# Kernel optimization log

Hardware: AMD Instinct MI355X
Metric: run time of the kernel (lower is better)

## Reference

```python
import jax, jax.numpy as jnp
import numpy as np

N, E, D, R = 50000, 800000, 128, 16
NUM_OBJS, NUM_ATTRS, L = 179, 10, 5
OBJ_DIM, ATTR_DIM, HID, NANGLE = 96, 32, 512, 24


def setup_inputs() -> dict:
    key = jax.random.key(0)
    ks = jax.random.split(key, 20)
    z = jax.random.normal(ks[0], (N, D), dtype=jnp.float32)
    objs = jax.random.randint(ks[1], (N,), 0, NUM_OBJS + 1)
    s = jax.random.randint(ks[2], (E,), 0, N)
    o = jax.random.randint(ks[3], (E,), 0, N)
    p = jax.random.randint(ks[4], (E,), 0, R)
    triples = jnp.stack([s, p, o], axis=1)
    attributes = jax.random.randint(ks[5], (N,), 0, NUM_ATTRS)
    w = 0.05
    obj_emb = jax.random.normal(ks[6], (NUM_OBJS + 1, OBJ_DIM), dtype=jnp.float32)
    attr_emb = jax.random.normal(ks[7], (NUM_ATTRS, ATTR_DIM), dtype=jnp.float32)
    Wrel = jax.random.normal(ks[8], (L, R, D, D), dtype=jnp.float32) * w
    Wroot = jax.random.normal(ks[9], (L, D, D), dtype=jnp.float32) * w
    bconv = jnp.zeros((L, D), dtype=jnp.float32)
    box_W1 = jax.random.normal(ks[10], (2 * D + ATTR_DIM, HID), dtype=jnp.float32) * w
    box_b1 = jnp.zeros((HID,), dtype=jnp.float32)
    box_W2 = jax.random.normal(ks[11], (HID, 6), dtype=jnp.float32) * w
    box_b2 = jnp.zeros((6,), dtype=jnp.float32)
    ang_W1 = jax.random.normal(ks[12], (2 * D, HID), dtype=jnp.float32) * w
    ang_b1 = jnp.zeros((HID,), dtype=jnp.float32)
    ang_W2 = jax.random.normal(ks[13], (HID, NANGLE), dtype=jnp.float32) * w
    ang_b2 = jnp.zeros((NANGLE,), dtype=jnp.float32)
    return dict(z=z, objs=objs, triples=triples, attributes=attributes,
                obj_emb=obj_emb, attr_emb=attr_emb, Wrel=Wrel, Wroot=Wroot,
                bconv=bconv, box_W1=box_W1, box_b1=box_b1, box_W2=box_W2,
                box_b2=box_b2, ang_W1=ang_W1, ang_b1=ang_b1, ang_W2=ang_W2,
                ang_b2=ang_b2)


def _rgcn_layer(x, s, o, p, Wr, Wroot_l, b):
    # relation-typed transform of all nodes: [N, R, D]
    h_rel = jnp.einsum('nd,rdf->nrf', x, Wr)
    msgs = h_rel[s, p]                                   # [E, D] gather
    # mean aggregation per (target, relation), as in PyG RGCNConv
    seg = o * R + p
    cnt = jax.ops.segment_sum(jnp.ones((s.shape[0],), x.dtype), seg,
                              num_segments=x.shape[0] * R)
    deg = jnp.maximum(cnt[seg], 1.0)
    agg = jax.ops.segment_sum(msgs / deg[:, None], o, num_segments=x.shape[0])
    return x @ Wroot_l + agg + b


def reference(z, objs, triples, attributes, obj_emb, attr_emb, Wrel, Wroot,
              bconv, box_W1, box_b1, box_W2, box_b2, ang_W1, ang_b1,
              ang_W2, ang_b2):
    s, p, o = triples[:, 0], triples[:, 1], triples[:, 2]
    attr_vecs = attr_emb[attributes]                     # [N, 32]
    obj_vecs = jnp.concatenate([obj_emb[objs], attr_vecs], axis=1)  # [N, 128]
    for j in range(L):
        obj_vecs = jax.nn.relu(_rgcn_layer(obj_vecs, s, o, p,
                                           Wrel[j], Wroot[j], bconv[j]))
    obj_vecs = jnp.concatenate([obj_vecs, z], axis=1)    # [N, 256]
    obj_vecs_box = jnp.concatenate([obj_vecs, attr_vecs], axis=1)  # [N, 288]
    boxes_pred = jax.nn.relu(obj_vecs_box @ box_W1 + box_b1) @ box_W2 + box_b2
    ang_h = jax.nn.relu(obj_vecs @ ang_W1 + ang_b1) @ ang_W2 + ang_b2
    angles_pred = jax.nn.log_softmax(ang_h, axis=1)
    return boxes_pred, angles_pred
```

## Files before the change

### kernel.cpp

```cpp
#include <hip/hip_runtime.h>
#include <hip/hip_bf16.h>
#include <math.h>

#define NN   50000
#define EE   800000
#define RREL 16
#define LLAY 5
#define NBINS (NN * RREL)
#define HCAP 565248

typedef __attribute__((ext_vector_type(8))) short s8v;
typedef __attribute__((ext_vector_type(4))) float f4v;

__device__ __forceinline__ unsigned short f2bf(float f) {
  __hip_bfloat16 h = __float2bfloat16(f);
  return __builtin_bit_cast(unsigned short, h);
}
__device__ __forceinline__ float bf2f(unsigned int u) {
  return __builtin_bit_cast(float, u << 16);
}
__device__ __forceinline__ void split1(float v, unsigned short& h, unsigned short& l) {
  __hip_bfloat16 hb = __float2bfloat16(v);
  float hf = __bfloat162float(hb);
  h = __builtin_bit_cast(unsigned short, hb);
  __hip_bfloat16 lb = __float2bfloat16(v - hf);
  l = __builtin_bit_cast(unsigned short, lb);
}

__global__ void build_x0_kernel(const int* __restrict__ objs, const int* __restrict__ attrs,
                                const float* __restrict__ obj_emb, const float* __restrict__ attr_emb,
                                unsigned short* __restrict__ xh) {
  int t = blockIdx.x * blockDim.x + threadIdx.x;
  if (t >= NN * 32) return;
  int n = t >> 5, q = t & 31;
  float4 v;
  if (q < 24) v = *(const float4*)&obj_emb[(size_t)objs[n] * 96 + q * 4];
  else        v = *(const float4*)&attr_emb[(size_t)attrs[n] * 32 + (q - 24) * 4];
  ushort4 h;
  h.x = f2bf(v.x); h.y = f2bf(v.y); h.z = f2bf(v.z); h.w = f2bf(v.w);
  *(ushort4*)&xh[(size_t)n * 128 + q * 4] = h;
}

__global__ void prep_zattr(const float* __restrict__ z, const int* __restrict__ attrs,
                           const float* __restrict__ attr_emb,
                           unsigned short* __restrict__ zh, unsigned short* __restrict__ ah) {
  int t = blockIdx.x * blockDim.x + threadIdx.x;
  if (t >= NN * 40) return;
  int n = t / 40, q = t % 40;
  float4 v;
  ushort4 h;
  if (q < 32) {
    v = *(const float4*)&z[(size_t)n * 128 + q * 4];
    h.x = f2bf(v.x); h.y = f2bf(v.y); h.z = f2bf(v.z); h.w = f2bf(v.w);
    *(ushort4*)&zh[(size_t)n * 128 + q * 4] = h;
  } else {
    int qq = q - 32;
    v = *(const float4*)&attr_emb[(size_t)attrs[n] * 32 + qq * 4];
    h.x = f2bf(v.x); h.y = f2bf(v.y); h.z = f2bf(v.z); h.w = f2bf(v.w);
    *(ushort4*)&ah[(size_t)n * 32 + qq * 4] = h;
  }
}

__global__ void count_kernel(const int* __restrict__ triples, int* __restrict__ cnt) {
  int e = blockIdx.x * 256 + threadIdx.x;
  if (e >= EE) return;
  int p = triples[e * 3 + 1], o = triples[e * 3 + 2];
  atomicAdd(&cnt[o * RREL + p], 1);
}
__global__ void scanA(const int* __restrict__ cnt, int* __restrict__ binStart,
                      int* __restrict__ partial) {
  __shared__ int buf[1024];
  int g = blockIdx.x * 1024 + threadIdx.x;
  int v = (g < NBINS) ? cnt[g] : 0;
  buf[threadIdx.x] = v;
  __syncthreads();
  for (int d = 1; d < 1024; d <<= 1) {
    int t = (threadIdx.x >= d) ? buf[threadIdx.x - d] : 0;
    __syncthreads();
    buf[threadIdx.x] += t;
    __syncthreads();
  }
  if (g < NBINS) binStart[g] = buf[threadIdx.x] - v;
  if (threadIdx.x == 1023) partial[blockIdx.x] = buf[1023];
}
__global__ void scanB(int* __restrict__ partial, int* __restrict__ binStart, int nPart) {
  __shared__ int buf[1024];
  int v = (threadIdx.x < nPart) ? partial[threadIdx.x] : 0;
  buf[threadIdx.x] = v;
  __syncthreads();
  for (int d = 1; d < 1024; d <<= 1) {
    int t = (threadIdx.x >= d) ? buf[threadIdx.x - d] : 0;
    __syncthreads();
    buf[threadIdx.x] += t;
    __syncthreads();
  }
  if (threadIdx.x < nPart) partial[threadIdx.x] = buf[threadIdx.x] - v;
  if (threadIdx.x == 1023) binStart[NBINS] = buf[1023];
}
__global__ void scanC(int* __restrict__ binStart, const int* __restrict__ partial) {
  int g = blockIdx.x * 1024 + threadIdx.x;
  if (g < NBINS) binStart[g] += partial[blockIdx.x];
}

__global__ void mark_cells(const int* __restrict__ triples, int* __restrict__ sMark) {
  int e = blockIdx.x * 256 + threadIdx.x;
  if (e >= EE) return;
  int s = triples[e * 3 + 0], p = triples[e * 3 + 1];
  atomicAdd(&sMark[s * RREL + p], 1);
}
__global__ void count_dp(const int* __restrict__ sMark, int* __restrict__ Dp) {
  __shared__ int lh[RREL];
  if (threadIdx.x < RREL) lh[threadIdx.x] = 0;
  __syncthreads();
  int c = blockIdx.x * 256 + threadIdx.x;
  if (c < NBINS && sMark[c] > 0) atomicAdd(&lh[c & 15], 1);
  __syncthreads();
  if (threadIdx.x < RREL && lh[threadIdx.x] > 0)
    atomicAdd(&Dp[threadIdx.x], lh[threadIdx.x]);
}
__global__ void pad_scan(const int* __restrict__ Dp, int* __restrict__ pStart) {
  if (threadIdx.x == 0 && blockIdx.x == 0) {
    int s = 0;
    for (int p = 0; p < RREL; ++p) {
      pStart[p] = s;
      s += ((Dp[p] + 127) >> 7) << 7;
    }
    pStart[RREL] = s;
  }
}
__global__ void assign_cells(int* __restrict__ sMark, const int* __restrict__ pStart,
                             int* __restrict__ pcur, int* __restrict__ spRel) {
  __shared__ int lh[RREL], lbase[RREL];
  if (threadIdx.x < RREL) lh[threadIdx.x] = 0;
  __syncthreads();
  int c = blockIdx.x * 256 + threadIdx.x;
  bool occ = (c < NBINS) && (sMark[c] > 0);
  int p = 0, my = 0;
  if (occ) { p = c & 15; my = atomicAdd(&lh[p], 1); }
  __syncthreads();
  if (threadIdx.x < RREL)
    lbase[threadIdx.x] = (lh[threadIdx.x] > 0)
                           ? atomicAdd(&pcur[threadIdx.x], lh[threadIdx.x]) : 0;
  __syncthreads();
  if (occ) {
    int cid = pStart[p] + lbase[p] + my;
    if (cid < HCAP) spRel[cid] = c;
    sMark[c] = cid + 1;
  }
}
__global__ void place_kernel(const int* __restrict__ triples, const int* __restrict__ cnt,
                             const int* __restrict__ binStart, int* __restrict__ cursor,
                             const int* __restrict__ sMark,
                             int* __restrict__ offD, float* __restrict__ wD) {
  int e = blockIdx.x * 256 + threadIdx.x;
  if (e >= EE) return;
  int s = triples[e * 3 + 0], p = triples[e * 3 + 1], o = triples[e * 3 + 2];
  int bin = o * RREL + p;
  int pos = binStart[bin] + atomicAdd(&cursor[bin], 1);
  int cid = sMark[s * RREL + p] - 1;
  offD[pos] = cid * 128;
  wD[pos] = 1.0f / (float)cnt[bin];
}

__global__ void prep_wrel(const float* __restrict__ Wrel, unsigned short* __restrict__ WThi,
                          unsigned short* __restrict__ WTlo) {
  int t = blockIdx.x * 256 + threadIdx.x;
  if (t >= LLAY * RREL * 128 * 128) return;
  int f = t & 127, k = (t >> 7) & 127, lr = t >> 14;
  float v = Wrel[((size_t)lr * 128 + k) * 128 + f];
  size_t di = ((size_t)lr * 128 + f) * 128 + k;
  split1(v, WThi[di], WTlo[di]);
}
__global__ void prep_wroot(const float* __restrict__ Wroot, unsigned short* __restrict__ hi,
                           unsigned short* __restrict__ lo) {
  int t = blockIdx.x * 256 + threadIdx.x;
  if (t >= LLAY * 128 * 128) return;
  int f = t & 127, k = (t >> 7) & 127, l = t >> 14;
  float v = Wroot[((size_t)l * 128 + k) * 128 + f];
  size_t di = ((size_t)l * 128 + f) * 128 + k;
  split1(v, hi[di], lo[di]);
}
__global__ void prep_wcat(const float* __restrict__ box_W1, const float* __restrict__ ang_W1,
                          unsigned short* __restrict__ hi, unsigned short* __restrict__ lo) {
  int t = blockIdx.x * 256 + threadIdx.x;
  if (t >= 1024 * 288) return;
  int k = t % 288, c = t / 288;
  float v;
  if (c < 512) v = box_W1[(size_t)k * 512 + c];
  else         v = (k < 256) ? ang_W1[(size_t)k * 512 + (c - 512)] : 0.f;
  split1(v, hi[(size_t)c * 288 + k], lo[(size_t)c * 288 + k]);
}
__global__ void prep_bcat(const float* __restrict__ box_b1, const float* __restrict__ ang_b1,
                          float* __restrict__ bcat) {
  int t = blockIdx.x * 256 + threadIdx.x;
  if (t >= 1024) return;
  bcat[t] = (t < 512) ? box_b1[t] : ang_b1[t - 512];
}
__global__ void prep_w2cat(const float* __restrict__ box_W2, const float* __restrict__ ang_W2,
                           unsigned short* __restrict__ hi, unsigned short* __restrict__ lo) {
  int t = blockIdx.x * 256 + threadIdx.x;
  if (t >= 32 * 1024) return;
  int k = t & 1023, c = t >> 10;
  float v = 0.f;
  if (c < 6)       { if (k < 512)  v = box_W2[(size_t)k * 6 + c]; }
  else if (c < 30) { if (k >= 512) v = ang_W2[(size_t)(k - 512) * 24 + (c - 6)]; }
  split1(v, hi[(size_t)c * 1024 + k], lo[(size_t)c * 1024 + k]);
}

__global__ __launch_bounds__(256) void hrelc_mfma(const unsigned short* __restrict__ xh,
                                                  const int* __restrict__ spRel,
                                                  const unsigned short* __restrict__ Wh,
                                                  const unsigned short* __restrict__ Wl,
                                                  unsigned short* __restrict__ Hc) {
  __shared__ __align__(16) unsigned short As[128][40];
  __shared__ __align__(16) unsigned short Bs[2][128][40];
  const int tid = threadIdx.x;
  const int row0 = blockIdx.x * 128;
  const int sr0 = spRel[row0];
  if (sr0 < 0) return;
  const int p = sr0 & 15;
  const unsigned short* WHp = Wh + (size_t)p * 128 * 128;
  const unsigned short* WLp = Wl + (size_t)p * 128 * 128;

  const int wid = tid >> 6, lane = tid & 63;
  const int rg = wid >> 1, cg = wid & 1;
  const int lr = lane & 15, lk = (lane >> 4) * 8;
  f4v acc[4][4] = {};

  const int ar = tid >> 1, ahalf = tid & 1;
  const int aspv = spRel[row0 + ar];
  const int arow = (aspv >= 0) ? (aspv >> 4) : -1;
  s8v aR0, aR1;
  s8v bR[4];

  auto loadStep = [&](int k0) {
    if (arow >= 0) {
      aR0 = *(const s8v*)&xh[(size_t)arow * 128 + k0 + ahalf * 16];
      aR1 = *(const s8v*)&xh[(size_t)arow * 128 + k0 + ahalf * 16 + 8];
    } else {
      s8v zz = {0,0,0,0,0,0,0,0}; aR0 = zz; aR1 = zz;
    }
#pragma unroll
    for (int i = 0; i < 4; ++i) {
      int idx = tid + i * 256;
      int hl = idx >> 9;
      int rem = idx & 511;
      int c = rem >> 2, c8 = (rem & 3) * 8;
      const unsigned short* Wp = hl ? WLp : WHp;
      bR[i] = *(const s8v*)&Wp[(size_t)c * 128 + k0 + c8];
    }
  };
  auto writeStep = [&]() {
    *(s8v*)&As[ar][ahalf * 16]     = aR0;
    *(s8v*)&As[ar][ahalf * 16 + 8] = aR1;
#pragma unroll
    for (int i = 0; i < 4; ++i) {
      int idx = tid + i * 256;
      int hl = idx >> 9;
      int rem = idx & 511;
      int c = rem >> 2, c8 = (rem & 3) * 8;
      *(s8v*)&Bs[hl][c][c8] = bR[i];
    }
  };

  loadStep(0);
  for (int k0 = 0; k0 < 128; k0 += 32) {
    __syncthreads();
    writeStep();
    __syncthreads();
    if (k0 < 96) loadStep(k0 + 32);

    s8v ah[4];
#pragma unroll
    for (int mf = 0; mf < 4; ++mf) ah[mf] = *(s8v*)&As[rg * 64 + mf * 16 + lr][lk];
#pragma unroll
    for (int nf = 0; nf < 4; ++nf) {
      s8v bh_ = *(s8v*)&Bs[0][cg * 64 + nf * 16 + lr][lk];
      s8v bl_ = *(s8v*)&Bs[1][cg * 64 + nf * 16 + lr][lk];
#pragma unroll
      for (int mf = 0; mf < 4; ++mf) {
        acc[mf][nf] = __builtin_amdgcn_mfma_f32_16x16x32_bf16(ah[mf], bh_, acc[mf][nf], 0, 0, 0);
        acc[mf][nf] = __builtin_amdgcn_mfma_f32_16x16x32_bf16(ah[mf], bl_, acc[mf][nf], 0, 0, 0);
      }
    }
  }

#pragma unroll
  for (int mf = 0; mf < 4; ++mf)
#pragma unroll
    for (int nf = 0; nf < 4; ++nf) {
      f4v v = acc[mf][nf];
      int rbase = row0 + rg * 64 + mf * 16 + (lane >> 4) * 4;
      int col = cg * 64 + nf * 16 + lr;
#pragma unroll
      for (int q = 0; q < 4; ++q)
        Hc[(size_t)(rbase + q) * 128 + col] = f2bf(v[q]);
    }
}

__global__ __launch_bounds__(256) void root_mfma(const unsigned short* __restrict__ xh,
                                                 const unsigned short* __restrict__ Bh,
                                                 const unsigned short* __restrict__ Bl,
                                                 const float* __restrict__ bias,
                                                 unsigned short* __restrict__ xr) {
  __shared__ __align__(16) unsigned short As[64][40];
  __shared__ __align__(16) unsigned short Bs[2][128][40];
  const int tid = threadIdx.x;
  const int row0 = blockIdx.x * 64;
  const int wid = tid >> 6, lane = tid & 63;
  const int lr = lane & 15, lk = (lane >> 4) * 8;
  const int wrow = (wid >> 1) * 32, wcol = (wid & 1) * 64;
  f4v acc[2][4] = {};

  s8v aR;
  s8v bR[4];
  const int ar = tid >> 2, ac8 = (tid & 3) * 8;
  const int an = row0 + ar;

  auto loadStep = [&](int k0) {
    if (an < NN) aR = *(const s8v*)&xh[(size_t)an * 128 + k0 + ac8];
    else { s8v zz = {0,0,0,0,0,0,0,0}; aR = zz; }
#pragma unroll
    for (int i = 0; i < 4; ++i) {
      int idx = tid + i * 256;
      int hl = idx >> 9;
      int rem = idx & 511;
      int c = rem >> 2, c8 = (rem & 3) * 8;
      const unsigned short* Wp = hl ? Bl : Bh;
      bR[i] = *(const s8v*)&Wp[(size_t)c * 128 + k0 + c8];
    }
  };
  auto writeStep = [&]() {
    *(s8v*)&As[ar][ac8] = aR;
#pragma unroll
    for (int i = 0; i < 4; ++i) {
      int idx = tid + i * 256;
      int hl = idx >> 9;
      int rem = idx & 511;
      int c = rem >> 2, c8 = (rem & 3) * 8;
      *(s8v*)&Bs[hl][c][c8] = bR[i];
    }
  };

  loadStep(0);
  for (int k0 = 0; k0 < 128; k0 += 32) {
    __syncthreads();
    writeStep();
    __syncthreads();
    if (k0 < 96) loadStep(k0 + 32);
#pragma unroll
    for (int mf = 0; mf < 2; ++mf) {
      s8v ah_ = *(s8v*)&As[wrow + mf * 16 + lr][lk];
#pragma unroll
      for (int nf = 0; nf < 4; ++nf) {
        s8v bh_ = *(s8v*)&Bs[0][wcol + nf * 16 + lr][lk];
        s8v bl_ = *(s8v*)&Bs[1][wcol + nf * 16 + lr][lk];
        acc[mf][nf] = __builtin_amdgcn_mfma_f32_16x16x32_bf16(ah_, bh_, acc[mf][nf], 0, 0, 0);
        acc[mf][nf] = __builtin_amdgcn_mfma_f32_16x16x32_bf16(ah_, bl_, acc[mf][nf], 0, 0, 0);
      }
    }
  }
#pragma unroll
  for (int mf = 0; mf < 2; ++mf)
#pragma unroll
    for (int nf = 0; nf < 4; ++nf) {
      int col = wcol + nf * 16 + lr;
      float b = bias[col];
      int rbase = row0 + wrow + mf * 16 + (lane >> 4) * 4;
#pragma unroll
      for (int q = 0; q < 4; ++q) {
        int rr = rbase + q;
        if (rr < NN) xr[(size_t)rr * 128 + col] = f2bf(acc[mf][nf][q] + b);
      }
    }
}

__global__ __launch_bounds__(256) void mlpcat_mfma(const unsigned short* __restrict__ xh,
                                                   const unsigned short* __restrict__ zh,
                                                   const unsigned short* __restrict__ ath,
                                                   const unsigned short* __restrict__ Wh,
                                                   const unsigned short* __restrict__ Wl,
                                                   const float* __restrict__ bcat,
                                                   unsigned short* __restrict__ H) {
  __shared__ __align__(16) unsigned short As[64][40];
  __shared__ __align__(16) unsigned short Bs[2][256][40];
  const int tid = threadIdx.x;
  const int row0 = blockIdx.y * 64;
  const int cb = blockIdx.x;
  const int wid = tid >> 6, lane = tid & 63;
  const int wcol = wid * 64;
  const int lr = lane & 15, lk = (lane >> 4) * 8;
  f4v acc[4][4] = {};

  s8v aR;
  s8v bR[8];
  const int ar = tid >> 2, ac8 = (tid & 3) * 8;
  const int an = row0 + ar;

  auto loadStep = [&](int k0) {
    if (an < NN) {
      if (k0 < 128)      aR = *(const s8v*)&xh[(size_t)an * 128 + k0 + ac8];
      else if (k0 < 256) aR = *(const s8v*)&zh[(size_t)an * 128 + (k0 - 128) + ac8];
      else               aR = *(const s8v*)&ath[(size_t)an * 32 + (k0 - 256) + ac8];
    } else { s8v zz = {0, 0, 0, 0, 0, 0, 0, 0}; aR = zz; }
#pragma unroll
    for (int i = 0; i < 8; ++i) {
      int idx = tid + i * 256;
      int hl = idx >> 10;
      int rem = idx & 1023;
      int c = rem >> 2, c8 = (rem & 3) * 8;
      int gc = cb * 256 + c;
      const unsigned short* Wp = hl ? Wl : Wh;
      bR[i] = *(const s8v*)&Wp[(size_t)gc * 288 + k0 + c8];
    }
  };
  auto writeStep = [&]() {
    *(s8v*)&As[ar][ac8] = aR;
#pragma unroll
    for (int i = 0; i < 8; ++i) {
      int idx = tid + i * 256;
      int hl = idx >> 10;
      int rem = idx & 1023;
      int c = rem >> 2, c8 = (rem & 3) * 8;
      *(s8v*)&Bs[hl][c][c8] = bR[i];
    }
  };

  loadStep(0);
  for (int step = 0; step < 9; ++step) {
    __syncthreads();
    writeStep();
    __syncthreads();
    if (step < 8) loadStep((step + 1) * 32);

    s8v ah[4];
#pragma unroll
    for (int mf = 0; mf < 4; ++mf) ah[mf] = *(s8v*)&As[mf * 16 + lr][lk];
#pragma unroll
    for (int nf = 0; nf < 4; ++nf) {
      s8v bh_ = *(s8v*)&Bs[0][wcol + nf * 16 + lr][lk];
      s8v bl_ = *(s8v*)&Bs[1][wcol + nf * 16 + lr][lk];
#pragma unroll
      for (int mf = 0; mf < 4; ++mf) {
        acc[mf][nf] = __builtin_amdgcn_mfma_f32_16x16x32_bf16(ah[mf], bh_, acc[mf][nf], 0, 0, 0);
        acc[mf][nf] = __builtin_amdgcn_mfma_f32_16x16x32_bf16(ah[mf], bl_, acc[mf][nf], 0, 0, 0);
      }
    }
  }
#pragma unroll
  for (int mf = 0; mf < 4; ++mf)
#pragma unroll
    for (int nf = 0; nf < 4; ++nf) {
      int gc = cb * 256 + wcol + nf * 16 + lr;
      float b = bcat[gc];
      int rbase = row0 + mf * 16 + (lane >> 4) * 4;
#pragma unroll
      for (int q = 0; q < 4; ++q) {
        int rr = rbase + q;
        if (rr < NN) H[(size_t)rr * 1024 + gc] = f2bf(fmaxf(acc[mf][nf][q] + b, 0.f));
      }
    }
}

__global__ __launch_bounds__(256) void head_mfma(const unsigned short* __restrict__ H,
                                                 const unsigned short* __restrict__ Wh,
                                                 const unsigned short* __restrict__ Wl,
                                                 float* __restrict__ logits) {
  __shared__ __align__(16) unsigned short As[256][40];
  __shared__ __align__(16) unsigned short Bs[2][32][40];
  const int tid = threadIdx.x;
  const int row0 = blockIdx.x * 256;
  const int wid = tid >> 6, lane = tid & 63;
  const int wrow = wid * 64;
  const int lr = lane & 15, lk = (lane >> 4) * 8;
  f4v acc[4][2] = {};

  s8v aR[4];
  s8v bR;
  const int br_hl = tid >> 7, br_rem = tid & 127;
  const int br_col = br_rem >> 2, br_c8 = (br_rem & 3) * 8;

  auto loadStep = [&](int k0) {
#pragma unroll
    for (int i = 0; i < 4; ++i) {
      int idx = tid + i * 256;
      int r = idx >> 2, c8 = (idx & 3) * 8;
      int n = row0 + r;
      if (n < NN) aR[i] = *(const s8v*)&H[(size_t)n * 1024 + k0 + c8];
      else { s8v zz = {0, 0, 0, 0, 0, 0, 0, 0}; aR[i] = zz; }
    }
    const unsigned short* Wp = br_hl ? Wl : Wh;
    bR = *(const s8v*)&Wp[(size_t)br_col * 1024 + k0 + br_c8];
  };
  auto writeStep = [&]() {
#pragma unroll
    for (int i = 0; i < 4; ++i) {
      int idx = tid + i * 256;
      int r = idx >> 2, c8 = (idx & 3) * 8;
      *(s8v*)&As[r][c8] = aR[i];
    }
    *(s8v*)&Bs[br_hl][br_col][br_c8] = bR;
  };

  loadStep(0);
  for (int step = 0; step < 32; ++step) {
    __syncthreads();
    writeStep();
    __syncthreads();
    if (step < 31) loadStep((step + 1) * 32);
#pragma unroll
    for (int nf = 0; nf < 2; ++nf) {
      s8v bh_ = *(s8v*)&Bs[0][nf * 16 + lr][lk];
      s8v bl_ = *(s8v*)&Bs[1][nf * 16 + lr][lk];
#pragma unroll
      for (int mf = 0; mf < 4; ++mf) {
        s8v a_ = *(s8v*)&As[wrow + mf * 16 + lr][lk];
        acc[mf][nf] = __builtin_amdgcn_mfma_f32_16x16x32_bf16(a_, bh_, acc[mf][nf], 0, 0, 0);
        acc[mf][nf] = __builtin_amdgcn_mfma_f32_16x16x32_bf16(a_, bl_, acc[mf][nf], 0, 0, 0);
      }
    }
  }
#pragma unroll
  for (int mf = 0; mf < 4; ++mf)
#pragma unroll
    for (int nf = 0; nf < 2; ++nf) {
      int col = nf * 16 + lr;
      int rbase = row0 + wrow + mf * 16 + (lane >> 4) * 4;
#pragma unroll
      for (int q = 0; q < 4; ++q) {
        int rr = rbase + q;
        if (rr < NN) logits[(size_t)rr * 32 + col] = acc[mf][nf][q];
      }
    }
}

__global__ void head_post(const float* __restrict__ logits, const float* __restrict__ box_b2,
                          const float* __restrict__ ang_b2, float* __restrict__ out) {
  int n = blockIdx.x * 256 + threadIdx.x;
  if (n >= NN) return;
  float l[32];
#pragma unroll
  for (int i = 0; i < 8; ++i)
    *(float4*)&l[i * 4] = *(const float4*)&logits[(size_t)n * 32 + i * 4];
  float* ob = out + (size_t)n * 6;
#pragma unroll
  for (int c = 0; c < 6; ++c) ob[c] = l[c] + box_b2[c];
  float a[24];
  float mx = -1e30f;
#pragma unroll
  for (int c = 0; c < 24; ++c) { a[c] = l[6 + c] + ang_b2[c]; mx = fmaxf(mx, a[c]); }
  float ssum = 0.f;
#pragma unroll
  for (int c = 0; c < 24; ++c) ssum += expf(a[c] - mx);
  float lse = mx + logf(ssum);
  float* oa = out + (size_t)NN * 6 + (size_t)n * 24;
#pragma unroll
  for (int c = 0; c < 24; ++c) oa[c] = a[c] - lse;
}

__global__ __launch_bounds__(256) void gather_kernel(const unsigned short* __restrict__ Hc,
                                                     const int* __restrict__ binStart,
                                                     const int* __restrict__ offD,
                                                     const float* __restrict__ wD,
                                                     const unsigned short* __restrict__ xr,
                                                     unsigned short* __restrict__ xh) {
  int wid = threadIdx.x >> 6, lane = threadIdx.x & 63;
  int o = blockIdx.x * 4 + wid;
  if (o >= NN) return;
  int beg = binStart[o * RREL];
  int end = binStart[o * RREL + RREL];
  float a0 = 0.f, a1 = 0.f, b0 = 0.f, b1 = 0.f;
  int i = beg;
  for (; i + 1 < end; i += 2) {
    int of1 = offD[i], of2 = offD[i + 1];
    float w1 = wD[i], w2 = wD[i + 1];
    unsigned int u1 = *(const unsigned int*)&Hc[of1 + lane * 2];
    unsigned int u2 = *(const unsigned int*)&Hc[of2 + lane * 2];
    a0 += w1 * bf2f(u1 & 0xffffu);
    a1 += w1 * bf2f(u1 >> 16);
    b0 += w2 * bf2f(u2 & 0xffffu);
    b1 += w2 * bf2f(u2 >> 16);
  }
  if (i < end) {
    int of1 = offD[i];
    float w1 = wD[i];
    unsigned int u1 = *(const unsigned int*)&Hc[of1 + lane * 2];
    a0 += w1 * bf2f(u1 & 0xffffu);
    a1 += w1 * bf2f(u1 >> 16);
  }
  a0 += b0; a1 += b1;
  unsigned int ur = *(const unsigned int*)&xr[(size_t)o * 128 + lane * 2];
  float c0 = bf2f(ur & 0xffffu) + a0;
  float c1 = bf2f(ur >> 16) + a1;
  c0 = fmaxf(c0, 0.f); c1 = fmaxf(c1, 0.f);
  unsigned int pk = (unsigned int)f2bf(c0) | ((unsigned int)f2bf(c1) << 16);
  *(unsigned int*)&xh[(size_t)o * 128 + lane * 2] = pk;
}

extern "C" void kernel_launch(void* const* d_in, const int* in_sizes, int n_in,
                              void* d_out, int out_size, void* d_ws, size_t ws_size,
                              hipStream_t stream) {
  const float* z        = (const float*)d_in[0];
  const int*   objs     = (const int*)d_in[1];
  const int*   triples  = (const int*)d_in[2];
  const int*   attrs    = (const int*)d_in[3];
  const float* obj_emb  = (const float*)d_in[4];
  const float* attr_emb = (const float*)d_in[5];
  const float* Wrel     = (const float*)d_in[6];
  const float* Wroot    = (const float*)d_in[7];
  const float* bconv    = (const float*)d_in[8];
  const float* box_W1   = (const float*)d_in[9];
  const float* box_b1   = (const float*)d_in[10];
  const float* box_W2   = (const float*)d_in[11];
  const float* box_b2   = (const float*)d_in[12];
  const float* ang_W1   = (const float*)d_in[13];
  const float* ang_b1   = (const float*)d_in[14];
  const float* ang_W2   = (const float*)d_in[15];
  const float* ang_b2   = (const float*)d_in[16];
  float* out = (float*)d_out;

  char* base = (char*)d_ws;
  size_t cur = 0;
  auto alloc = [&](size_t bytes) -> char* {
    char* p = base + cur;
    cur += (bytes + 255) & ~(size_t)255;
    return p;
  };
  unsigned short* Hc   = (unsigned short*)alloc((size_t)HCAP * 128 * 2);
  unsigned short* xr   = (unsigned short*)alloc((size_t)NN * 128 * 2);
  unsigned short* xhi  = (unsigned short*)alloc((size_t)NN * 128 * 2);
  unsigned short* zhi  = (unsigned short*)alloc((size_t)NN * 128 * 2);
  unsigned short* athi = (unsigned short*)alloc((size_t)NN * 32 * 2);
  unsigned short* WThi = (unsigned short*)alloc((size_t)LLAY * RREL * 128 * 128 * 2);
  unsigned short* WTlo = (unsigned short*)alloc((size_t)LLAY * RREL * 128 * 128 * 2);
  unsigned short* WrtH = (unsigned short*)alloc((size_t)LLAY * 128 * 128 * 2);
  unsigned short* WrtL = (unsigned short*)alloc((size_t)LLAY * 128 * 128 * 2);
  unsigned short* WcH  = (unsigned short*)alloc((size_t)1024 * 288 * 2);
  unsigned short* WcL  = (unsigned short*)alloc((size_t)1024 * 288 * 2);
  unsigned short* W2H  = (unsigned short*)alloc((size_t)32 * 1024 * 2);
  unsigned short* W2L  = (unsigned short*)alloc((size_t)32 * 1024 * 2);
  float* bcat          = (float*)alloc(1024 * 4);
  float* logits        = (float*)alloc((size_t)NN * 32 * 4);
  int*   cnt      = (int*)alloc((size_t)NBINS * 4);
  int*   binStart = (int*)alloc((size_t)(NBINS + 1) * 4);
  int*   cursor   = (int*)alloc((size_t)NBINS * 4);
  int*   sMark    = (int*)alloc((size_t)NBINS * 4);
  int*   spRel    = (int*)alloc((size_t)HCAP * 4);
  int*   partial  = (int*)alloc(4096);
  int*   meta     = (int*)alloc(256);
  int*   offD     = (int*)alloc((size_t)EE * 4);
  float* wD       = (float*)alloc((size_t)EE * 4);
  int* Dp = meta, *pStart = meta + 16, *pcur = meta + 40;
  unsigned short* Hmlp = Hc;

  hipMemsetAsync(cnt, 0, (size_t)NBINS * 4, stream);
  hipMemsetAsync(cursor, 0, (size_t)NBINS * 4, stream);
  hipMemsetAsync(sMark, 0, (size_t)NBINS * 4, stream);
  hipMemsetAsync(meta, 0, 256, stream);
  hipMemsetAsync(spRel, 0xFF, (size_t)HCAP * 4, stream);

  build_x0_kernel<<<(NN * 32 + 255) / 256, 256, 0, stream>>>(objs, attrs, obj_emb, attr_emb, xhi);
  prep_zattr<<<(NN * 40 + 255) / 256, 256, 0, stream>>>(z, attrs, attr_emb, zhi, athi);
  count_kernel<<<(EE + 255) / 256, 256, 0, stream>>>(triples, cnt);
  const int nPart = (NBINS + 1023) / 1024;
  scanA<<<nPart, 1024, 0, stream>>>(cnt, binStart, partial);
  scanB<<<1, 1024, 0, stream>>>(partial, binStart, nPart);
  scanC<<<nPart, 1024, 0, stream>>>(binStart, partial);
  mark_cells<<<(EE + 255) / 256, 256, 0, stream>>>(triples, sMark);
  count_dp<<<(NBINS + 255) / 256, 256, 0, stream>>>(sMark, Dp);
  pad_scan<<<1, 64, 0, stream>>>(Dp, pStart);
  assign_cells<<<(NBINS + 255) / 256, 256, 0, stream>>>(sMark, pStart, pcur, spRel);
  place_kernel<<<(EE + 255) / 256, 256, 0, stream>>>(triples, cnt, binStart, cursor, sMark,
                                                     offD, wD);
  prep_wrel<<<(LLAY * RREL * 128 * 128 + 255) / 256, 256, 0, stream>>>(Wrel, WThi, WTlo);
  prep_wroot<<<(LLAY * 128 * 128 + 255) / 256, 256, 0, stream>>>(Wroot, WrtH, WrtL);
  prep_wcat<<<(1024 * 288 + 255) / 256, 256, 0, stream>>>(box_W1, ang_W1, WcH, WcL);
  prep_bcat<<<4, 256, 0, stream>>>(box_b1, ang_b1, bcat);
  prep_w2cat<<<(32 * 1024 + 255) / 256, 256, 0, stream>>>(box_W2, ang_W2, W2H, W2L);

  const int rowBlocks = (NN + 63) / 64;
  for (int j = 0; j < LLAY; ++j) {
    root_mfma<<<rowBlocks, 256, 0, stream>>>(xhi, WrtH + (size_t)j * 128 * 128,
                                             WrtL + (size_t)j * 128 * 128,
                                             bconv + (size_t)j * 128, xr);
    hrelc_mfma<<<HCAP / 128, 256, 0, stream>>>(xhi, spRel,
                                               WThi + (size_t)j * RREL * 128 * 128,
                                               WTlo + (size_t)j * RREL * 128 * 128, Hc);
    gather_kernel<<<(NN + 3) / 4, 256, 0, stream>>>(Hc, binStart, offD, wD, xr, xhi);
  }

  mlpcat_mfma<<<dim3(4, rowBlocks), 256, 0, stream>>>(xhi, zhi, athi, WcH, WcL, bcat, Hmlp);
  head_mfma<<<(NN + 255) / 256, 256, 0, stream>>>(Hmlp, W2H, W2L, logits);
  head_post<<<(NN + 255) / 256, 256, 0, stream>>>(logits, box_b2, ang_b2, out);
}
```

Measured before the change: 1.009 ms.

## Fold root transform into relation GEMM and widen MLP tile to 128 rows

```diff
diff --git a/kernel.cpp b/kernel.cpp
--- a/kernel.cpp
+++ b/kernel.cpp
@@ -126,6 +126,8 @@
       s += ((Dp[p] + 127) >> 7) << 7;
     }
     pStart[RREL] = s;
+    s += ((NN + 127) >> 7) << 7;
+    pStart[RREL + 1] = s;
   }
 }
 __global__ void assign_cells(int* __restrict__ sMark, const int* __restrict__ pStart,
@@ -144,9 +146,15 @@
   __syncthreads();
   if (occ) {
     int cid = pStart[p] + lbase[p] + my;
-    if (cid < HCAP) spRel[cid] = c;
+    if (cid < HCAP) spRel[cid] = (c >> 4) * 32 + p;
     sMark[c] = cid + 1;
   }
+}
+__global__ void fill_root(const int* __restrict__ pStart, int* __restrict__ spRel) {
+  int n = blockIdx.x * 256 + threadIdx.x;
+  if (n >= NN) return;
+  int cid = pStart[RREL] + n;
+  if (cid < HCAP) spRel[cid] = n * 32 + 16;
 }
 __global__ void place_kernel(const int* __restrict__ triples, const int* __restrict__ cnt,
                              const int* __restrict__ binStart, int* __restrict__ cursor,
@@ -211,16 +219,22 @@
                                                   const int* __restrict__ spRel,
                                                   const unsigned short* __restrict__ Wh,
                                                   const unsigned short* __restrict__ Wl,
-                                                  unsigned short* __restrict__ Hc) {
+                                                  const unsigned short* __restrict__ Rh,
+                                                  const unsigned short* __restrict__ Rl,
+                                                  const float* __restrict__ bias,
+                                                  const int* __restrict__ pStart,
+                                                  unsigned short* __restrict__ Hc,
+                                                  unsigned short* __restrict__ xr) {
   __shared__ __align__(16) unsigned short As[128][40];
   __shared__ __align__(16) unsigned short Bs[2][128][40];
   const int tid = threadIdx.x;
   const int row0 = blockIdx.x * 128;
   const int sr0 = spRel[row0];
   if (sr0 < 0) return;
-  const int p = sr0 & 15;
-  const unsigned short* WHp = Wh + (size_t)p * 128 * 128;
-  const unsigned short* WLp = Wl + (size_t)p * 128 * 128;
+  const int p = sr0 & 31;
+  const bool isRoot = (p == 16);
+  const unsigned short* WHp = isRoot ? Rh : Wh + (size_t)p * 128 * 128;
+  const unsigned short* WLp = isRoot ? Rl : Wl + (size_t)p * 128 * 128;
 
   const int wid = tid >> 6, lane = tid & 63;
   const int rg = wid >> 1, cg = wid & 1;
@@ -229,7 +243,7 @@
 
   const int ar = tid >> 1, ahalf = tid & 1;
   const int aspv = spRel[row0 + ar];
-  const int arow = (aspv >= 0) ? (aspv >> 4) : -1;
+  const int arow = (aspv >= 0) ? (aspv >> 5) : -1;
   s8v aR0, aR1;
   s8v bR[4];
 
@@ -285,115 +299,57 @@
     }
   }
 
-#pragma unroll
-  for (int mf = 0; mf < 4; ++mf)
-#pragma unroll
-    for (int nf = 0; nf < 4; ++nf) {
-      f4v v = acc[mf][nf];
-      int rbase = row0 + rg * 64 + mf * 16 + (lane >> 4) * 4;
-      int col = cg * 64 + nf * 16 + lr;
-#pragma unroll
-      for (int q = 0; q < 4; ++q)
-        Hc[(size_t)(rbase + q) * 128 + col] = f2bf(v[q]);
-    }
-}
-
-__global__ __launch_bounds__(256) void root_mfma(const unsigned short* __restrict__ xh,
-                                                 const unsigned short* __restrict__ Bh,
-                                                 const unsigned short* __restrict__ Bl,
-                                                 const float* __restrict__ bias,
-                                                 unsigned short* __restrict__ xr) {
-  __shared__ __align__(16) unsigned short As[64][40];
-  __shared__ __align__(16) unsigned short Bs[2][128][40];
-  const int tid = threadIdx.x;
-  const int row0 = blockIdx.x * 64;
-  const int wid = tid >> 6, lane = tid & 63;
-  const int lr = lane & 15, lk = (lane >> 4) * 8;
-  const int wrow = (wid >> 1) * 32, wcol = (wid & 1) * 64;
-  f4v acc[2][4] = {};
-
-  s8v aR;
-  s8v bR[4];
-  const int ar = tid >> 2, ac8 = (tid & 3) * 8;
-  const int an = row0 + ar;
-
-  auto loadStep = [&](int k0) {
-    if (an < NN) aR = *(const s8v*)&xh[(size_t)an * 128 + k0 + ac8];
-    else { s8v zz = {0,0,0,0,0,0,0,0}; aR = zz; }
-#pragma unroll
-    for (int i = 0; i < 4; ++i) {
-      int idx = tid + i * 256;
-      int hl = idx >> 9;
-      int rem = idx & 511;
-      int c = rem >> 2, c8 = (rem & 3) * 8;
-      const unsigned short* Wp = hl ? Bl : Bh;
-      bR[i] = *(const s8v*)&Wp[(size_t)c * 128 + k0 + c8];
-    }
-  };
-  auto writeStep = [&]() {
-    *(s8v*)&As[ar][ac8] = aR;
-#pragma unroll
-    for (int i = 0; i < 4; ++i) {
-      int idx = tid + i * 256;
-      int hl = idx >> 9;
-      int rem = idx & 511;
-      int c = rem >> 2, c8 = (rem & 3) * 8;
-      *(s8v*)&Bs[hl][c][c8] = bR[i];
-    }
-  };
-
-  loadStep(0);
-  for (int k0 = 0; k0 < 128; k0 += 32) {
-    __syncthreads();
-    writeStep();
-    __syncthreads();
-    if (k0 < 96) loadStep(k0 + 32);
-#pragma unroll
-    for (int mf = 0; mf < 2; ++mf) {
-      s8v ah_ = *(s8v*)&As[wrow + mf * 16 + lr][lk];
+  if (!isRoot) {
+#pragma unroll
+    for (int mf = 0; mf < 4; ++mf)
 #pragma unroll
       for (int nf = 0; nf < 4; ++nf) {
-        s8v bh_ = *(s8v*)&Bs[0][wcol + nf * 16 + lr][lk];
-        s8v bl_ = *(s8v*)&Bs[1][wcol + nf * 16 + lr][lk];
-        acc[mf][nf] = __builtin_amdgcn_mfma_f32_16x16x32_bf16(ah_, bh_, acc[mf][nf], 0, 0, 0);
-        acc[mf][nf] = __builtin_amdgcn_mfma_f32_16x16x32_bf16(ah_, bl_, acc[mf][nf], 0, 0, 0);
+        f4v v = acc[mf][nf];
+        int rbase = row0 + rg * 64 + mf * 16 + (lane >> 4) * 4;
+        int col = cg * 64 + nf * 16 + lr;
+#pragma unroll
+        for (int q = 0; q < 4; ++q)
+          Hc[(size_t)(rbase + q) * 128 + col] = f2bf(v[q]);
       }
-    }
-  }
-#pragma unroll
-  for (int mf = 0; mf < 2; ++mf)
-#pragma unroll
-    for (int nf = 0; nf < 4; ++nf) {
-      int col = wcol + nf * 16 + lr;
-      float b = bias[col];
-      int rbase = row0 + wrow + mf * 16 + (lane >> 4) * 4;
-#pragma unroll
-      for (int q = 0; q < 4; ++q) {
-        int rr = rbase + q;
-        if (rr < NN) xr[(size_t)rr * 128 + col] = f2bf(acc[mf][nf][q] + b);
+  } else {
+    const int rootBase = pStart[RREL];
+#pragma unroll
+    for (int mf = 0; mf < 4; ++mf)
+#pragma unroll
+      for (int nf = 0; nf < 4; ++nf) {
+        f4v v = acc[mf][nf];
+        int rbase = row0 + rg * 64 + mf * 16 + (lane >> 4) * 4;
+        int col = cg * 64 + nf * 16 + lr;
+        float b = bias[col];
+#pragma unroll
+        for (int q = 0; q < 4; ++q) {
+          int node = rbase + q - rootBase;
+          if (node >= 0 && node < NN)
+            xr[(size_t)node * 128 + col] = f2bf(v[q] + b);
+        }
       }
-    }
-}
-
-__global__ __launch_bounds__(256) void mlpcat_mfma(const unsigned short* __restrict__ xh,
+  }
+}
+
+__global__ __launch_bounds__(512) void mlpcat_mfma(const unsigned short* __restrict__ xh,
                                                    const unsigned short* __restrict__ zh,
                                                    const unsigned short* __restrict__ ath,
                                                    const unsigned short* __restrict__ Wh,
                                                    const unsigned short* __restrict__ Wl,
                                                    const float* __restrict__ bcat,
                                                    unsigned short* __restrict__ H) {
-  __shared__ __align__(16) unsigned short As[64][40];
+  __shared__ __align__(16) unsigned short As[128][40];
   __shared__ __align__(16) unsigned short Bs[2][256][40];
   const int tid = threadIdx.x;
-  const int row0 = blockIdx.y * 64;
+  const int row0 = blockIdx.y * 128;
   const int cb = blockIdx.x;
   const int wid = tid >> 6, lane = tid & 63;
-  const int wcol = wid * 64;
+  const int wrow = (wid >> 2) * 64, wcol = (wid & 3) * 64;
   const int lr = lane & 15, lk = (lane >> 4) * 8;
   f4v acc[4][4] = {};
 
   s8v aR;
-  s8v bR[8];
+  s8v bR[4];
   const int ar = tid >> 2, ac8 = (tid & 3) * 8;
   const int an = row0 + ar;
 
@@ -404,8 +360,8 @@
       else               aR = *(const s8v*)&ath[(size_t)an * 32 + (k0 - 256) + ac8];
     } else { s8v zz = {0, 0, 0, 0, 0, 0, 0, 0}; aR = zz; }
 #pragma unroll
-    for (int i = 0; i < 8; ++i) {
-      int idx = tid + i * 256;
+    for (int i = 0; i < 4; ++i) {
+      int idx = tid + i * 512;
       int hl = idx >> 10;
       int rem = idx & 1023;
       int c = rem >> 2, c8 = (rem & 3) * 8;
@@ -417,8 +373,8 @@
   auto writeStep = [&]() {
     *(s8v*)&As[ar][ac8] = aR;
 #pragma unroll
-    for (int i = 0; i < 8; ++i) {
-      int idx = tid + i * 256;
+    for (int i = 0; i < 4; ++i) {
+      int idx = tid + i * 512;
       int hl = idx >> 10;
       int rem = idx & 1023;
       int c = rem >> 2, c8 = (rem & 3) * 8;
@@ -435,7 +391,7 @@
 
     s8v ah[4];
 #pragma unroll
-    for (int mf = 0; mf < 4; ++mf) ah[mf] = *(s8v*)&As[mf * 16 + lr][lk];
+    for (int mf = 0; mf < 4; ++mf) ah[mf] = *(s8v*)&As[wrow + mf * 16 + lr][lk];
 #pragma unroll
     for (int nf = 0; nf < 4; ++nf) {
       s8v bh_ = *(s8v*)&Bs[0][wcol + nf * 16 + lr][lk];
@@ -453,7 +409,7 @@
     for (int nf = 0; nf < 4; ++nf) {
       int gc = cb * 256 + wcol + nf * 16 + lr;
       float b = bcat[gc];
-      int rbase = row0 + mf * 16 + (lane >> 4) * 4;
+      int rbase = row0 + wrow + mf * 16 + (lane >> 4) * 4;
 #pragma unroll
       for (int q = 0; q < 4; ++q) {
         int rr = rbase + q;
@@ -670,6 +626,7 @@
   count_dp<<<(NBINS + 255) / 256, 256, 0, stream>>>(sMark, Dp);
   pad_scan<<<1, 64, 0, stream>>>(Dp, pStart);
   assign_cells<<<(NBINS + 255) / 256, 256, 0, stream>>>(sMark, pStart, pcur, spRel);
+  fill_root<<<(NN + 255) / 256, 256, 0, stream>>>(pStart, spRel);
   place_kernel<<<(EE + 255) / 256, 256, 0, stream>>>(triples, cnt, binStart, cursor, sMark,
                                                      offD, wD);
   prep_wrel<<<(LLAY * RREL * 128 * 128 + 255) / 256, 256, 0, stream>>>(Wrel, WThi, WTlo);
@@ -678,18 +635,17 @@
   prep_bcat<<<4, 256, 0, stream>>>(box_b1, ang_b1, bcat);
   prep_w2cat<<<(32 * 1024 + 255) / 256, 256, 0, stream>>>(box_W2, ang_W2, W2H, W2L);
 
-  const int rowBlocks = (NN + 63) / 64;
   for (int j = 0; j < LLAY; ++j) {
-    root_mfma<<<rowBlocks, 256, 0, stream>>>(xhi, WrtH + (size_t)j * 128 * 128,
-                                             WrtL + (size_t)j * 128 * 128,
-                                             bconv + (size_t)j * 128, xr);
     hrelc_mfma<<<HCAP / 128, 256, 0, stream>>>(xhi, spRel,
                                                WThi + (size_t)j * RREL * 128 * 128,
-                                               WTlo + (size_t)j * RREL * 128 * 128, Hc);
+                                               WTlo + (size_t)j * RREL * 128 * 128,
+                                               WrtH + (size_t)j * 128 * 128,
+                                               WrtL + (size_t)j * 128 * 128,
+                                               bconv + (size_t)j * 128, pStart, Hc, xr);
     gather_kernel<<<(NN + 3) / 4, 256, 0, stream>>>(Hc, binStart, offD, wD, xr, xhi);
   }
 
-  mlpcat_mfma<<<dim3(4, rowBlocks), 256, 0, stream>>>(xhi, zhi, athi, WcH, WcL, bcat, Hmlp);
+  mlpcat_mfma<<<dim3(4, (NN + 127) / 128), 512, 0, stream>>>(xhi, zhi, athi, WcH, WcL, bcat, Hmlp);
   head_mfma<<<(NN + 255) / 256, 256, 0, stream>>>(Hmlp, W2H, W2L, logits);
   head_post<<<(NN + 255) / 256, 256, 0, stream>>>(logits, box_b2, ang_b2, out);
 }
```

Measured after the change: 1.007 ms. No clear change (-0.2%).
